# Performance work log

Hardware: AMD Instinct MI355X
Metric: run time of the kernel (lower is better)

The kernel has to match this reference:

```python
import jax, jax.numpy as jnp
import numpy as np

N_NODES = 50000      # nodes
N_EDGES = 800000     # edges (avg degree 16)
D = 128              # input_dim == hidden_dim
C = 32               # output_dim (classes)
G = 64               # number of graphs in batch
EPS = 1e-5           # LayerNorm eps (torch default)
NUM_LAYERS = 3


def setup_inputs() -> dict:
    key = jax.random.key(0)
    ks = jax.random.split(key, 12)
    scale = 1.0 / np.sqrt(D)
    x = jax.random.normal(ks[0], (N_NODES, D), dtype=jnp.float32)
    edge_index = jax.random.randint(ks[1], (2, N_EDGES), 0, N_NODES)
    batch = jnp.sort(jax.random.randint(ks[2], (N_NODES,), 0, G))
    # CustomConv params: self-loop linear + message linear, 3 layers stacked
    W_self = jax.random.normal(ks[3], (NUM_LAYERS, D, D), dtype=jnp.float32) * scale
    b_self = jnp.zeros((NUM_LAYERS, D), dtype=jnp.float32)
    W_msg = jax.random.normal(ks[4], (NUM_LAYERS, D, D), dtype=jnp.float32) * scale
    b_msg = jnp.zeros((NUM_LAYERS, D), dtype=jnp.float32)
    # two LayerNorms (after layers 0 and 1)
    ln_g = jnp.ones((2, D), dtype=jnp.float32)
    ln_b = jnp.zeros((2, D), dtype=jnp.float32)
    # post-MP MLP head: Linear(D,D) -> Dropout(identity in eval) -> Linear(D,C)
    W1 = jax.random.normal(ks[5], (D, D), dtype=jnp.float32) * scale
    b1 = jnp.zeros((D,), dtype=jnp.float32)
    W2 = jax.random.normal(ks[6], (D, C), dtype=jnp.float32) * scale
    b2 = jnp.zeros((C,), dtype=jnp.float32)
    return {"x": x, "W_self": W_self, "b_self": b_self, "W_msg": W_msg,
            "b_msg": b_msg, "ln_g": ln_g, "ln_b": ln_b, "W1": W1, "b1": b1,
            "W2": W2, "b2": b2, "edge_index": edge_index, "batch": batch}


def _layer_norm(h, g, b):
    mu = jnp.mean(h, axis=-1, keepdims=True)
    var = jnp.mean(jnp.square(h - mu), axis=-1, keepdims=True)
    return g * (h - mu) * jax.lax.rsqrt(var + EPS) + b


def reference(x, W_self, b_self, W_msg, b_msg, ln_g, ln_b, W1, b1, W2, b2,
              edge_index, batch):
    src, dst = edge_index[0], edge_index[1]
    for i in range(NUM_LAYERS):
        # CustomConv: self linear + sum-aggregated neighbor messages
        msg = x @ W_msg[i] + b_msg[i]                     # [N, D]
        agg = jax.ops.segment_sum(msg[src], dst, num_segments=N_NODES)
        x = x @ W_self[i] + b_self[i] + agg               # [N, D]
        x = jax.nn.relu(x)
        # dropout p=0.25 is identity in eval mode
        if i != NUM_LAYERS - 1:
            x = _layer_norm(x, ln_g[i], ln_b[i])
    # global mean pool over graphs
    sums = jax.ops.segment_sum(x, batch, num_segments=G)          # [G, D]
    cnt = jax.ops.segment_sum(jnp.ones((N_NODES,), x.dtype), batch,
                              num_segments=G)                     # [G]
    pooled = sums / jnp.maximum(cnt, 1.0)[:, None]
    # post-MP head (dropout identity in eval)
    h = pooled @ W1 + b1
    logits = h @ W2 + b2                                          # [G, C]
    return jax.nn.log_softmax(logits, axis=1)
```

## Files before the change

### kernel.cpp

```cpp
#include <hip/hip_runtime.h>
#include <hip/hip_bf16.h>
#include <math.h>

#define N_NODES 50000
#define N_EDGES 800000
#define DIM 128
#define CLS 32
#define NGRAPH 64
#define LN_EPS 1e-5f
#define NBLK 196
#define ABLK 256
#define EPB (N_EDGES / ABLK)
#define EB_STRIDE 7168
#define LCAP 8192
#define ROWS1 (N_NODES + 1)
#define CHK 4
#define CW 32
#define NPW 4
#define NPB2 (16 * NPW)
#define NCB ((N_NODES + NPB2 - 1) / NPB2)
#define SLOTH ((NCB + 1) / 2)
#define NPAD (NCB * NPB2)

typedef __attribute__((ext_vector_type(8))) short bf16x8;
typedef __attribute__((ext_vector_type(4))) float f32x4;
typedef __attribute__((ext_vector_type(2))) unsigned int u32x2;

static __device__ __forceinline__ int lower_bound_i(const int* a, int n, int key) {
    int lo = 0, hi = n;
    while (lo < hi) { int mid = (lo + hi) >> 1; if (a[mid] < key) lo = mid + 1; else hi = mid; }
    return lo;
}

static __device__ __forceinline__ void acc4(float* ac, u32x2 v) {
    union { unsigned int b; float f; } lo0, hi0, lo1, hi1;
    lo0.b = v.x << 16;
    hi0.b = v.x & 0xffff0000u;
    lo1.b = v.y << 16;
    hi1.b = v.y & 0xffff0000u;
    ac[0] += lo0.f;
    ac[1] += hi0.f;
    ac[2] += lo1.f;
    ac[3] += hi1.f;
}


__global__ __launch_bounds__(256) void prep_kernel(
    const float* __restrict__ x, const float* __restrict__ Wself,
    const float* __restrict__ Wmsg, __hip_bfloat16* __restrict__ XbIn,
    __hip_bfloat16* __restrict__ WTf,
    int* __restrict__ ecur, float* __restrict__ gsum,
    int* __restrict__ off, int* __restrict__ offe,
    __hip_bfloat16* __restrict__ padA, __hip_bfloat16* __restrict__ padB,
    __hip_bfloat16* __restrict__ padC, __hip_bfloat16* __restrict__ padD) {
    int i = blockIdx.x * 256 + threadIdx.x;
    if (i < N_NODES * DIM / 2) {
        float2 v = ((const float2*)x)[i];
        int n = i >> 6, kk = i & 63;
        int c = kk >> 4;
        __hip_bfloat162 hv = __float22bfloat162_rn(v);
        __builtin_nontemporal_store(*(unsigned int*)&hv,
            (unsigned int*)XbIn + ((size_t)c * ROWS1 + n) * 16 + (kk & 15));
    }
    if (i < 3 * 32768) {
        int l = i >> 15;
        int rem = i & 32767;
        int half = rem >> 14;
        int rem2 = rem & 16383;
        int ct = rem2 >> 11;
        int ks = (rem2 >> 9) & 3;
        int lane = (rem2 >> 3) & 63;
        int e = rem2 & 7;
        int q = lane >> 4, l15 = lane & 15;
        int n = ct * 16 + l15;
        int k = half * 128 + ks * 32 + q * 8 + e;
        float v = (k < 128) ? Wself[l * 16384 + k * 128 + n]
                            : Wmsg[l * 16384 + (k - 128) * 128 + n];
        WTf[i] = __float2bfloat16(v);
    }
    if (i < NBLK) ecur[i] = i * EB_STRIDE;
    if (i < NGRAPH * DIM) gsum[i] = 0.f;
    if (i >= N_NODES && i < NPAD) { off[i] = 0; offe[i] = 0; }
    if (i < 4 * CHK * CW) {
        __hip_bfloat16* bufs[4] = {padA, padB, padC, padD};
        int buf = i >> 7, c = (i >> 5) & 3, e = i & 31;
        bufs[buf][((size_t)c * ROWS1 + N_NODES) * CW + e] = __float2bfloat16(0.f);
    }
}


__global__ __launch_bounds__(1024) void bucket_kernel(
    const int* __restrict__ esrc, const int* __restrict__ edst,
    int* __restrict__ ecur, int* __restrict__ ebuf) {
    __shared__ int bc4[4][NBLK];
    __shared__ int bc[NBLK], bres[NBLK], bcnt[NBLK];
    const int t = threadIdx.x;
    const int e0 = blockIdx.x * EPB;
    for (int i = t; i < 4 * NBLK; i += 1024) ((int*)bc4)[i] = 0;
    __syncthreads();
    int dr[4], sr[4];
#pragma unroll
    for (int it = 0; it < 4; it++) {
        int i = t + it * 1024;
        if (i < EPB) { dr[it] = edst[e0 + i]; sr[it] = esrc[e0 + i]; }
        else { dr[it] = -1; sr[it] = 0; }
    }
    const int cpy = (t >> 6) & 3;
#pragma unroll
    for (int it = 0; it < 4; it++)
        if (dr[it] >= 0) atomicAdd(&bc4[cpy][dr[it] >> 8], 1);
    __syncthreads();
    if (t < NBLK) {
        int c = bc4[0][t] + bc4[1][t] + bc4[2][t] + bc4[3][t];
        int r = (c + 7) & ~7;
        int res = atomicAdd(&ecur[t], r);
        bres[t] = res;
        bcnt[t] = c;
        bc[t] = res;
    }
    __syncthreads();
#pragma unroll
    for (int it = 0; it < 4; it++)
        if (dr[it] >= 0) {
            int d = dr[it];
            int pos = atomicAdd(&bc[d >> 8], 1);
            ebuf[pos] = ((d & 255) << 16) | sr[it];
        }
    __syncthreads();
    if (t < NBLK) {
        int c = bcnt[t], r = (c + 7) & ~7, base = bres[t];
        for (int j = c; j < r; j++) ebuf[base + j] = -1;
    }
}


__global__ __launch_bounds__(1024) void csr_fused_kernel(
    const int* __restrict__ ebuf, const int* __restrict__ ecur,
    int* __restrict__ counts, int* __restrict__ off, int* __restrict__ offe,
    unsigned short* __restrict__ csr) {
    __shared__ int ncnt[256];
    __shared__ int ssc[256];
    __shared__ int cur[256];
    __shared__ unsigned short lcsr[LCAP];
    const int b = blockIdx.x, t = threadIdx.x;
    const int used = ecur[b] - b * EB_STRIDE;
    const int* eb = ebuf + b * EB_STRIDE;
    for (int i = t; i < LCAP / 2; i += 1024)
        ((unsigned int*)lcsr)[i] = 0xC350C350u;
    if (t < 256) ncnt[t] = 0;
    __syncthreads();
    for (int i = t; i < used; i += 1024) {
        int p = eb[i];
        if (p != -1) atomicAdd(&ncnt[p >> 16], 1);
    }
    __syncthreads();
    int myc = 0, mypad = 0;
    const int gi = b * 256 + t;
    if (t < 256) {
        myc = (gi < N_NODES) ? ncnt[t] : 0;
        mypad = (myc + 7) & ~7;
        ssc[t] = mypad;
    }
    __syncthreads();
    for (int o = 1; o < 256; o <<= 1) {
        int v = 0;
        if (t < 256 && t >= o) v = ssc[t - o];
        __syncthreads();
        if (t < 256) ssc[t] += v;
        __syncthreads();
    }
    if (t < 256) {
        int eoff = ssc[t] - mypad;
        cur[t] = eoff;
        if (gi < N_NODES) {
            off[gi] = b * LCAP + eoff;
            offe[gi] = b * LCAP + eoff + mypad;
            counts[gi] = myc;
        }
    }
    __syncthreads();
    for (int i = t; i < used; i += 1024) {
        int p = eb[i];
        if (p != -1) {
            int pos = atomicAdd(&cur[p >> 16], 1);
            lcsr[pos] = (unsigned short)(p & 0xFFFF);
        }
    }
    __syncthreads();
    const int total = ssc[255];
    int4* dst4 = (int4*)(csr + (size_t)b * LCAP);
    const int4* src4 = (const int4*)lcsr;
    for (int i = t; i < (total >> 3); i += 1024) dst4[i] = src4[i];
}


__global__ __launch_bounds__(1024) void agg_kernel(
    const __hip_bfloat16* __restrict__ Xg, const int* __restrict__ off,
    const int* __restrict__ offe, const unsigned short* __restrict__ csr,
    __hip_bfloat16* __restrict__ Sg) {
    const int b = blockIdx.x;
    const int slot = b & 7;
    const int chunk = slot & 3;
    const int half = slot >> 2;
    const int nbidx = (b >> 3) * 2 + half;
    const int w = __builtin_amdgcn_readfirstlane(threadIdx.x >> 6);
    const int lane = threadIdx.x & 63;
    const int l8 = lane & 7, g8 = lane >> 3;
    const char* X = (const char*)(Xg + (size_t)chunk * ROWS1 * CW);
    const int nbase = nbidx * NPB2 + w * NPW;
    const int loff = l8 * 8;
    const int coff = g8 * 4;

    int bj[NPW], ej[NPW];
    float ac[NPW][4];
#pragma unroll
    for (int j = 0; j < NPW; j++) {
        int n = nbase + j;
        bj[j] = off[n];
        ej[j] = offe[n];
        ac[j][0] = ac[j][1] = ac[j][2] = ac[j][3] = 0.f;
    }
    for (;;) {
        int act = 0;
#pragma unroll
        for (int j = 0; j < NPW; j++) act |= (bj[j] + 16 <= ej[j]) ? (1 << j) : 0;
        if (!act) break;
        unsigned int u[NPW];
#pragma unroll
        for (int j = 0; j < NPW; j++)
            if (act & (1 << j))
                u[j] = *(const unsigned int*)((const char*)(csr + bj[j]) + coff);
        u32x2 v0[NPW], v1[NPW];
#pragma unroll
        for (int j = 0; j < NPW; j++)
            if (act & (1 << j)) {
                int s0 = u[j] & 0xffff, s1 = u[j] >> 16;
                v0[j] = *(const u32x2*)(X + ((s0 << 6) | loff));
                v1[j] = *(const u32x2*)(X + ((s1 << 6) | loff));
            }
#pragma unroll
        for (int j = 0; j < NPW; j++)
            if (act & (1 << j)) {
                acc4(ac[j], v0[j]);
                acc4(ac[j], v1[j]);
                bj[j] += 16;
            }
    }
    {
        unsigned int u[NPW];
        int tact = 0;
#pragma unroll
        for (int j = 0; j < NPW; j++)
            if (bj[j] < ej[j]) {
                tact |= (1 << j);
                u[j] = csr[bj[j] + g8];
            }
#pragma unroll
        for (int j = 0; j < NPW; j++)
            if (tact & (1 << j)) {
                u32x2 v = *(const u32x2*)(X + (((int)u[j] << 6) | loff));
                acc4(ac[j], v);
            }
    }
#pragma unroll
    for (int j = 0; j < NPW; j++)
#pragma unroll
        for (int k = 0; k < 4; k++) {
            ac[j][k] += __shfl_xor(ac[j][k], 8, 64);
            ac[j][k] += __shfl_xor(ac[j][k], 16, 64);
            ac[j][k] += __shfl_xor(ac[j][k], 32, 64);
        }
    if (lane < 8) {
#pragma unroll
        for (int j = 0; j < NPW; j++) {
            int n = nbase + j;
            if (n < N_NODES) {
                union { u32x2 u; __hip_bfloat162 h[2]; } pk;
                pk.h[0] = __float22bfloat162_rn(make_float2(ac[j][0], ac[j][1]));
                pk.h[1] = __float22bfloat162_rn(make_float2(ac[j][2], ac[j][3]));
                __builtin_nontemporal_store(pk.u,
                    (u32x2*)(Sg + ((size_t)chunk * ROWS1 + n) * CW + lane * 4));
            }
        }
    }
}


__global__ __launch_bounds__(256) void layer_mfma_kernel(
    const __hip_bfloat16* __restrict__ Xg, const __hip_bfloat16* __restrict__ Sg,
    const __hip_bfloat16* __restrict__ WTf,
    const float* __restrict__ bself, const float* __restrict__ bmsg,
    const int* __restrict__ counts,
    const float* __restrict__ lng, const float* __restrict__ lnb,
    const int* __restrict__ batch, float* __restrict__ gsum,
    __hip_bfloat16* __restrict__ Xout, int do_ln, int do_pool) {
    __shared__ __hip_bfloat16 wlds[16384];
    const int tid = threadIdx.x;
    const int w = tid >> 6, lane = tid & 63;
    const int l15 = lane & 15, q = lane >> 4;
    const int growbase = blockIdx.x * 64 + w * 16;
    const int row = growbase + l15;
    const int rowc = min(row, N_NODES);

    f32x4 acc[8];
#pragma unroll
    for (int ct = 0; ct < 8; ct++) acc[ct] = (f32x4){0.f, 0.f, 0.f, 0.f};

    {
        const uint4* src = (const uint4*)WTf;
        uint4* dst = (uint4*)wlds;
#pragma unroll
        for (int i = 0; i < 8; i++) dst[tid + i * 256] = src[tid + i * 256];
    }
    __syncthreads();
#pragma unroll
    for (int ks = 0; ks < 4; ks++) {
        bf16x8 afrag = *(const bf16x8*)(Xg + ((size_t)ks * ROWS1 + rowc) * CW + q * 8);
#pragma unroll
        for (int ct = 0; ct < 8; ct++) {
            bf16x8 bfrag = *(const bf16x8*)(&wlds[(((ct * 4 + ks) * 64) + lane) * 8]);
            acc[ct] = __builtin_amdgcn_mfma_f32_16x16x32_bf16(afrag, bfrag, acc[ct], 0, 0, 0);
        }
    }
    __syncthreads();
    {
        const uint4* src = (const uint4*)(WTf + 16384);
        uint4* dst = (uint4*)wlds;
#pragma unroll
        for (int i = 0; i < 8; i++) dst[tid + i * 256] = src[tid + i * 256];
    }
    __syncthreads();
#pragma unroll
    for (int ks = 0; ks < 4; ks++) {
        bf16x8 afrag = *(const bf16x8*)(Sg + ((size_t)ks * ROWS1 + rowc) * CW + q * 8);
#pragma unroll
        for (int ct = 0; ct < 8; ct++) {
            bf16x8 bfrag = *(const bf16x8*)(&wlds[(((ct * 4 + ks) * 64) + lane) * 8]);
            acc[ct] = __builtin_amdgcn_mfma_f32_16x16x32_bf16(afrag, bfrag, acc[ct], 0, 0, 0);
        }
    }

    float racc[8];
#pragma unroll
    for (int ct = 0; ct < 8; ct++) racc[ct] = 0.f;
    int gw = 0;
    bool fastp = false;
    if (do_pool) {
        int first = (growbase < N_NODES) ? growbase : (N_NODES - 1);
        gw = batch[first];
        int lastrow = growbase + 15;
        fastp = (growbase < N_NODES) && (lastrow < N_NODES) && (batch[lastrow] == gw);
    }
#pragma unroll
    for (int r = 0; r < 4; r++) {
        int grow = growbase + q * 4 + r;
        bool valid = grow < N_NODES;
        float dg = valid ? (float)counts[grow] : 0.f;
        float v[8];
        float s1 = 0.f;
#pragma unroll
        for (int ct = 0; ct < 8; ct++) {
            int col = ct * 16 + l15;
            float h = acc[ct][r] + bself[col] + dg * bmsg[col];
            h = fmaxf(h, 0.f);
            v[ct] = h;
            s1 += h;
        }
        if (do_ln) {
#pragma unroll
            for (int m = 1; m < 16; m <<= 1) s1 += __shfl_xor(s1, m, 64);
            float mu = s1 * (1.0f / 128.0f);
            float s2 = 0.f;
#pragma unroll
            for (int ct = 0; ct < 8; ct++) { float d = v[ct] - mu; s2 += d * d; }
#pragma unroll
            for (int m = 1; m < 16; m <<= 1) s2 += __shfl_xor(s2, m, 64);
            float rs = rsqrtf(s2 * (1.0f / 128.0f) + LN_EPS);
#pragma unroll
            for (int ct = 0; ct < 8; ct++) {
                int col = ct * 16 + l15;
                v[ct] = lng[col] * (v[ct] - mu) * rs + lnb[col];
            }
        }
        if (do_pool) {
            if (fastp) {
#pragma unroll
                for (int ct = 0; ct < 8; ct++) racc[ct] += v[ct];
            } else if (valid) {
                int g = batch[grow];
#pragma unroll
                for (int ct = 0; ct < 8; ct++)
                    atomicAdd(&gsum[g * DIM + ct * 16 + l15], v[ct]);
            }
        } else if (valid) {
#pragma unroll
            for (int ct = 0; ct < 8; ct++) {
                __hip_bfloat16 hv = __float2bfloat16(v[ct]);
                __builtin_nontemporal_store(*(unsigned short*)&hv,
                    (unsigned short*)Xout +
                        ((size_t)(ct >> 1) * ROWS1 + grow) * CW + (ct & 1) * 16 + l15);
            }
        }
    }
    if (do_pool && fastp) {
#pragma unroll
        for (int ct = 0; ct < 8; ct++) {
            racc[ct] += __shfl_xor(racc[ct], 16, 64);
            racc[ct] += __shfl_xor(racc[ct], 32, 64);
        }
        if (q == 0) {
#pragma unroll
            for (int ct = 0; ct < 8; ct++)
                atomicAdd(&gsum[gw * DIM + ct * 16 + l15], racc[ct]);
        }
    }
}


__global__ __launch_bounds__(128) void head_kernel(
    const float* __restrict__ gsum, const int* __restrict__ batch,
    const float* __restrict__ W1, const float* __restrict__ b1,
    const float* __restrict__ W2, const float* __restrict__ b2,
    float* __restrict__ out) {
    __shared__ float p[128];
    __shared__ float hh[128];
    int g = blockIdx.x;
    int j = threadIdx.x;
    int lo = lower_bound_i(batch, N_NODES, g);
    int hi = lower_bound_i(batch, N_NODES, g + 1);
    float cnt = fmaxf((float)(hi - lo), 1.0f);
    p[j] = gsum[g * DIM + j] / cnt;
    __syncthreads();
    float s = b1[j];
    for (int k = 0; k < DIM; k++) s += p[k] * W1[k * DIM + j];
    hh[j] = s;
    __syncthreads();
    if (j < CLS) {
        float l = b2[j];
        for (int k = 0; k < DIM; k++) l += hh[k] * W2[k * CLS + j];
        float mx = l;
#pragma unroll
        for (int m = 16; m >= 1; m >>= 1) mx = fmaxf(mx, __shfl_xor(mx, m, 64));
        float ex = expf(l - mx);
        float se = ex;
#pragma unroll
        for (int m = 16; m >= 1; m >>= 1) se += __shfl_xor(se, m, 64);
        out[g * CLS + j] = l - mx - logf(se);
    }
}


extern "C" void kernel_launch(void* const* d_in, const int* in_sizes, int n_in,
                              void* d_out, int out_size, void* d_ws, size_t ws_size,
                              hipStream_t stream) {
    (void)in_sizes; (void)n_in; (void)out_size; (void)ws_size;
    const float* x     = (const float*)d_in[0];
    const float* Wself = (const float*)d_in[1];
    const float* bself = (const float*)d_in[2];
    const float* Wmsg  = (const float*)d_in[3];
    const float* bmsg  = (const float*)d_in[4];
    const float* lng   = (const float*)d_in[5];
    const float* lnb   = (const float*)d_in[6];
    const float* W1    = (const float*)d_in[7];
    const float* b1    = (const float*)d_in[8];
    const float* W2    = (const float*)d_in[9];
    const float* b2    = (const float*)d_in[10];
    const int*   ei    = (const int*)d_in[11];
    const int*   batch = (const int*)d_in[12];
    const int* esrc = ei;
    const int* edst = ei + N_EDGES;

    char* w = (char*)d_ws;
    size_t o = 0;
    auto alloc = [&](size_t bytes) { void* p = w + o; o += (bytes + 255) & ~(size_t)255; return p; };
    const size_t XSZ = (size_t)CHK * ROWS1 * CW * 2;
    __hip_bfloat16* XbIn = (__hip_bfloat16*)alloc(XSZ);
    __hip_bfloat16* Xb0  = (__hip_bfloat16*)alloc(XSZ);
    __hip_bfloat16* Xb1  = (__hip_bfloat16*)alloc(XSZ);
    __hip_bfloat16* Sg   = (__hip_bfloat16*)alloc(XSZ);
    __hip_bfloat16* WTf  = (__hip_bfloat16*)alloc((size_t)3 * 32768 * 2);
    int*   counts = (int*)alloc((size_t)N_NODES * 4);
    int*   offs   = (int*)alloc((size_t)NPAD * 4);
    int*   offe   = (int*)alloc((size_t)NPAD * 4);
    int*   ecur   = (int*)alloc((size_t)NBLK * 4);
    int*   ebuf   = (int*)alloc((size_t)NBLK * EB_STRIDE * 4);
    unsigned short* csr = (unsigned short*)alloc((size_t)NBLK * LCAP * 2);
    float* gsum   = (float*)alloc((size_t)NGRAPH * DIM * 4);

    prep_kernel<<<(N_NODES * DIM / 2 + 255) / 256, 256, 0, stream>>>(
        x, Wself, Wmsg, XbIn, WTf, ecur, gsum, offs, offe, XbIn, Xb0, Xb1, Sg);

    bucket_kernel<<<ABLK, 1024, 0, stream>>>(esrc, edst, ecur, ebuf);
    csr_fused_kernel<<<NBLK, 1024, 0, stream>>>(ebuf, ecur, counts, offs, offe, csr);

    const __hip_bfloat16* XbCur = XbIn;
    __hip_bfloat16* bbufs[3] = {Xb0, Xb1, Xb0};
    for (int i = 0; i < 3; i++) {
        agg_kernel<<<8 * SLOTH, 1024, 0, stream>>>(XbCur, offs, offe, csr, Sg);
        layer_mfma_kernel<<<(N_NODES + 63) / 64, 256, 0, stream>>>(
            XbCur, Sg, WTf + (size_t)i * 32768,
            bself + i * DIM, bmsg + i * DIM, counts,
            (i < 2) ? lng + i * DIM : lng, (i < 2) ? lnb + i * DIM : lnb,
            batch, gsum,
            bbufs[i], (i < 2) ? 1 : 0, (i == 2) ? 1 : 0);
        XbCur = bbufs[i];
    }

    head_kernel<<<NGRAPH, 128, 0, stream>>>(gsum, batch, W1, b1, W2, b2, (float*)d_out);
}
```

Measured before the change: 281.7 us.

## Shrink agg blocks to 256 threads and prefetch 32-edge CSR chunks

The aggregation kernel now launches 256-thread blocks (4 waves) instead of 1024, which gives many more, smaller blocks. Its inner loop now covers 32 edges per step: each lane loads 4 source indices at once, the next chunk's indices are software-prefetched before the current chunk is accumulated, and a 16-edge plus scalar tail handles the remainder. The aim is more memory-level parallelism and hidden index-load latency in the gather. The cost is higher register pressure and more code paths. NPAD is now hardcoded to 50048, which is assumed to cover the padded node count.

After: 278.4 us. About the same (-1.2%).

```diff
diff --git a/kernel.cpp b/kernel.cpp
--- a/kernel.cpp
+++ b/kernel.cpp
@@ -17,10 +17,11 @@
 #define CHK 4
 #define CW 32
 #define NPW 4
-#define NPB2 (16 * NPW)
-#define NCB ((N_NODES + NPB2 - 1) / NPB2)
-#define SLOTH ((NCB + 1) / 2)
-#define NPAD (NCB * NPB2)
+#define NPAD 50048
+#define AGG_WPB 4
+#define AGG_NPB (AGG_WPB * NPW)
+#define AGG_NCB ((N_NODES + AGG_NPB - 1) / AGG_NPB)
+#define AGG_SLOT ((AGG_NCB + 1) / 2)
 
 typedef __attribute__((ext_vector_type(8))) short bf16x8;
 typedef __attribute__((ext_vector_type(4))) float f32x4;
@@ -194,7 +195,7 @@
 }
 
 
-__global__ __launch_bounds__(1024) void agg_kernel(
+__global__ __launch_bounds__(256) void agg_kernel(
     const __hip_bfloat16* __restrict__ Xg, const int* __restrict__ off,
     const int* __restrict__ offe, const unsigned short* __restrict__ csr,
     __hip_bfloat16* __restrict__ Sg) {
@@ -207,9 +208,11 @@
     const int lane = threadIdx.x & 63;
     const int l8 = lane & 7, g8 = lane >> 3;
     const char* X = (const char*)(Xg + (size_t)chunk * ROWS1 * CW);
-    const int nbase = nbidx * NPB2 + w * NPW;
+    const char* C = (const char*)csr;
+    const int nbase = nbidx * AGG_NPB + w * NPW;
     const int loff = l8 * 8;
-    const int coff = g8 * 4;
+    const int c2off = g8 * 8;
+    const int c1off = g8 * 4;
 
     int bj[NPW], ej[NPW];
     float ac[NPW][4];
@@ -220,45 +223,83 @@
         ej[j] = offe[n];
         ac[j][0] = ac[j][1] = ac[j][2] = ac[j][3] = 0.f;
     }
-    for (;;) {
-        int act = 0;
-#pragma unroll
-        for (int j = 0; j < NPW; j++) act |= (bj[j] + 16 <= ej[j]) ? (1 << j) : 0;
-        if (!act) break;
-        unsigned int u[NPW];
-#pragma unroll
-        for (int j = 0; j < NPW; j++)
-            if (act & (1 << j))
-                u[j] = *(const unsigned int*)((const char*)(csr + bj[j]) + coff);
-        u32x2 v0[NPW], v1[NPW];
+
+    u32x2 u[NPW];
+    int act = 0;
+#pragma unroll
+    for (int j = 0; j < NPW; j++)
+        if (bj[j] + 32 <= ej[j]) {
+            act |= (1 << j);
+            u[j] = *(const u32x2*)(C + bj[j] * 2 + c2off);
+        }
+    while (act) {
+        u32x2 v0[NPW], v1[NPW], v2[NPW], v3[NPW];
 #pragma unroll
         for (int j = 0; j < NPW; j++)
             if (act & (1 << j)) {
-                int s0 = u[j] & 0xffff, s1 = u[j] >> 16;
+                int s0 = u[j].x & 0xffff, s1 = u[j].x >> 16;
+                int s2 = u[j].y & 0xffff, s3 = u[j].y >> 16;
                 v0[j] = *(const u32x2*)(X + ((s0 << 6) | loff));
                 v1[j] = *(const u32x2*)(X + ((s1 << 6) | loff));
+                v2[j] = *(const u32x2*)(X + ((s2 << 6) | loff));
+                v3[j] = *(const u32x2*)(X + ((s3 << 6) | loff));
+            }
+        int nact = 0;
+        u32x2 un[NPW];
+#pragma unroll
+        for (int j = 0; j < NPW; j++)
+            if (act & (1 << j)) {
+                bj[j] += 32;
+                if (bj[j] + 32 <= ej[j]) {
+                    nact |= (1 << j);
+                    un[j] = *(const u32x2*)(C + bj[j] * 2 + c2off);
+                }
             }
 #pragma unroll
         for (int j = 0; j < NPW; j++)
             if (act & (1 << j)) {
                 acc4(ac[j], v0[j]);
                 acc4(ac[j], v1[j]);
+                acc4(ac[j], v2[j]);
+                acc4(ac[j], v3[j]);
+            }
+#pragma unroll
+        for (int j = 0; j < NPW; j++) u[j] = un[j];
+        act = nact;
+    }
+    {
+        unsigned int ut[NPW];
+        int tact = 0;
+#pragma unroll
+        for (int j = 0; j < NPW; j++)
+            if (bj[j] + 16 <= ej[j]) {
+                tact |= (1 << j);
+                ut[j] = *(const unsigned int*)(C + bj[j] * 2 + c1off);
+            }
+#pragma unroll
+        for (int j = 0; j < NPW; j++)
+            if (tact & (1 << j)) {
+                int s0 = ut[j] & 0xffff, s1 = ut[j] >> 16;
+                u32x2 a = *(const u32x2*)(X + ((s0 << 6) | loff));
+                u32x2 c = *(const u32x2*)(X + ((s1 << 6) | loff));
+                acc4(ac[j], a);
+                acc4(ac[j], c);
                 bj[j] += 16;
             }
     }
     {
-        unsigned int u[NPW];
+        unsigned int ut[NPW];
         int tact = 0;
 #pragma unroll
         for (int j = 0; j < NPW; j++)
             if (bj[j] < ej[j]) {
                 tact |= (1 << j);
-                u[j] = csr[bj[j] + g8];
+                ut[j] = csr[bj[j] + g8];
             }
 #pragma unroll
         for (int j = 0; j < NPW; j++)
             if (tact & (1 << j)) {
-                u32x2 v = *(const u32x2*)(X + (((int)u[j] << 6) | loff));
+                u32x2 v = *(const u32x2*)(X + (((int)ut[j] << 6) | loff));
                 acc4(ac[j], v);
             }
     }
@@ -496,7 +537,7 @@
     const __hip_bfloat16* XbCur = XbIn;
     __hip_bfloat16* bbufs[3] = {Xb0, Xb1, Xb0};
     for (int i = 0; i < 3; i++) {
-        agg_kernel<<<8 * SLOTH, 1024, 0, stream>>>(XbCur, offs, offe, csr, Sg);
+        agg_kernel<<<8 * AGG_SLOT, 256, 0, stream>>>(XbCur, offs, offe, csr, Sg);
         layer_mfma_kernel<<<(N_NODES + 63) / 64, 256, 0, stream>>>(
             XbCur, Sg, WTf + (size_t)i * 32768,
             bself + i * DIM, bmsg + i * DIM, counts,
```
